# Kernel optimization log

Hardware: AMD Instinct MI355X
Metric: run time of the kernel (lower is better)

The kernel has to match this reference:

```python
import jax, jax.numpy as jnp
import numpy as np

N_STATE = 16
PNAMES = ['in_w', 'conv_w', 'conv_b', 'xproj_w', 'dt_w', 'dt_b', 'A_log', 'D', 'ln_g', 'ln_b', 'out_w']


def _ss2d_params(key, dm, K):
    di = 2 * dm                       # expand = 2
    dr = (dm + 15) // 16              # dt_rank = ceil(d_model/16)
    ks = jax.random.split(key, 6)
    s = lambda k, shape, sc: jax.random.normal(k, shape, jnp.float32) * sc
    cshape = (di, 1, 3, 3) if K == 4 else (di, 1, 3)   # depthwise conv kernel
    return {
        'in_w': s(ks[0], (2 * di, dm), dm ** -0.5),
        'conv_w': s(ks[1], cshape, 0.3),
        'conv_b': jnp.zeros((di,), jnp.float32),
        'xproj_w': s(ks[2], (K, dr + 2 * N_STATE, di), di ** -0.5),
        'dt_w': s(ks[3], (K, di, dr), dr ** -0.5),
        'dt_b': s(ks[4], (K, di), 0.1),
        'A_log': jnp.log(jnp.arange(1, N_STATE + 1, dtype=jnp.float32)) * jnp.ones((K, di, N_STATE), jnp.float32),
        'D': jnp.ones((K, di), jnp.float32),
        'ln_g': jnp.ones((di,), jnp.float32),
        'ln_b': jnp.zeros((di,), jnp.float32),
        'out_w': s(ks[5], (dm, di), di ** -0.5),
    }


def _ln(x, g, b, eps=1e-5):
    m = jnp.mean(x, -1, keepdims=True)
    v = jnp.mean((x - m) ** 2, -1, keepdims=True)
    return (x - m) * jax.lax.rsqrt(v + eps) * g + b


def _scan_branches(xs, p):
    # xs: (B, K, di, L) -- selective scan along L for each direction k
    dr = p['dt_w'].shape[-1]
    x_dbl = jnp.einsum('bkdl,kcd->bkcl', xs, p['xproj_w'])
    dts, Bs, Cs = jnp.split(x_dbl, [dr, dr + N_STATE], axis=2)
    delta = jax.nn.softplus(jnp.einsum('bkrl,kdr->bkdl', dts, p['dt_w']) + p['dt_b'][None, :, :, None])
    A = -jnp.exp(p['A_log'])                               # (K, di, N)
    dA = jnp.exp(jnp.einsum('bkdl,kdn->lbkdn', delta, A))  # time-major for scan
    dBu = jnp.einsum('bkdl,bknl,bkdl->lbkdn', delta, Bs, xs)

    def step(h, io):
        a, bu = io
        h = a * h + bu
        return h, h

    h0 = jnp.zeros(dA.shape[1:], xs.dtype)
    _, hs = jax.lax.scan(step, h0, (dA, dBu))              # (L, B, K, di, N)
    y = jnp.einsum('lbkdn,bknl->bkdl', hs, Cs)
    return y + xs * p['D'][None, :, :, None]


def _ss2d_2d(x, p):
    # VMamba SS2D: x (B, H, W, dm) -> (B, H, W, dm), 4 scan directions
    xz = jnp.einsum('bhwc,ec->bhwe', x, p['in_w'])
    xin, z = jnp.split(xz, 2, -1)
    u = xin.transpose(0, 3, 1, 2)
    u = jax.lax.conv_general_dilated(u, p['conv_w'], (1, 1), 'SAME',
        dimension_numbers=('NCHW', 'OIHW', 'NCHW'), feature_group_count=u.shape[1])
    u = jax.nn.silu(u + p['conv_b'][None, :, None, None])
    Bb, di, H, W = u.shape
    L = H * W
    xf = u.reshape(Bb, di, L)                              # row-major
    xt = u.transpose(0, 1, 3, 2).reshape(Bb, di, L)        # col-major
    xs = jnp.stack([xf, xt, xf[..., ::-1], xt[..., ::-1]], 1)
    ys = _scan_branches(xs, p)                             # (B, 4, di, L)
    y0 = ys[:, 0]
    y2 = ys[:, 2][..., ::-1]
    y1 = ys[:, 1].reshape(Bb, di, W, H).transpose(0, 1, 3, 2).reshape(Bb, di, L)
    y3 = ys[:, 3][..., ::-1].reshape(Bb, di, W, H).transpose(0, 1, 3, 2).reshape(Bb, di, L)
    y = (y0 + y1 + y2 + y3).transpose(0, 2, 1).reshape(Bb, H, W, di)
    y = _ln(y, p['ln_g'], p['ln_b']) * jax.nn.silu(z)
    return jnp.einsum('bhwe,ce->bhwc', y, p['out_w'])


def _ss2d_1d(x, p):
    # SS2D_xb fuse block: x (B, L, dm) -> (B, L, dm), bidirectional 1D scan
    xz = jnp.einsum('blc,ec->ble', x, p['in_w'])
    xin, z = jnp.split(xz, 2, -1)
    u = xin.transpose(0, 2, 1)
    u = jax.lax.conv_general_dilated(u, p['conv_w'], (1,), 'SAME',
        dimension_numbers=('NCH', 'OIH', 'NCH'), feature_group_count=u.shape[1])
    u = jax.nn.silu(u + p['conv_b'][None, :, None])
    xs = jnp.stack([u, u[..., ::-1]], 1)                   # K = 2
    ys = _scan_branches(xs, p)
    y = (ys[:, 0] + ys[:, 1][..., ::-1]).transpose(0, 2, 1)
    y = _ln(y, p['ln_g'], p['ln_b']) * jax.nn.silu(z)
    return jnp.einsum('ble,ce->blc', y, p['out_w'])


def _bridge(C1, C2, C3, p1, p2, p3, pf, n1_g, n1_b):
    y1 = _ss2d_2d(C1.transpose(0, 2, 3, 1), p1).transpose(0, 3, 1, 2)
    y2 = _ss2d_2d(C2.transpose(0, 2, 3, 1), p2).transpose(0, 3, 1, 2)
    y3 = _ss2d_2d(C3.transpose(0, 2, 3, 1), p3).transpose(0, 3, 1, 2)
    B_, C, H, W = y1.shape                                 # C=24, H=W=112
    # faithful RAW reshapes (no permute), exactly as the torch source does
    F1 = y1.reshape(B_, H * W, C)
    F2 = y2.reshape(B_, H * W // 2, C)
    F3 = y3.reshape(B_, H * W // 4, C)
    F = jnp.concatenate([F1, F2, F3], axis=1)              # (B, 21952, 24)
    F = F + _ss2d_1d(_ln(F, n1_g, n1_b), pf)               # dropout = identity (eval)
    o1 = F[:, :12544, :].reshape(B_, C, H, W)
    o2 = F[:, 12544:18816, :].reshape(B_, C * 2, H // 2, W // 2)
    o3 = F[:, 18816:, :].reshape(B_, C * 4, H // 4, W // 4)
    return (o1, o2, o3)


def setup_inputs() -> dict:
    key = jax.random.key(0)
    ks = jax.random.split(key, 7)
    inp = {
        'C1': jax.random.normal(ks[0], (1, 24, 112, 112), jnp.float32),
        'C2': jax.random.normal(ks[1], (1, 48, 56, 56), jnp.float32),
        'C3': jax.random.normal(ks[2], (1, 96, 28, 28), jnp.float32),
    }
    for pfx, dm, K, kk in [('m1', 24, 4, ks[3]), ('m2', 48, 4, ks[4]), ('m3', 96, 4, ks[5]), ('fz', 24, 2, ks[6])]:
        p = _ss2d_params(kk, dm, K)
        for n in PNAMES:
            inp[pfx + '_' + n] = p[n]
    inp['n1_g'] = jnp.ones((24,), jnp.float32)
    inp['n1_b'] = jnp.zeros((24,), jnp.float32)
    return inp


def reference(C1, C2, C3, m1_in_w, m1_conv_w, m1_conv_b, m1_xproj_w, m1_dt_w, m1_dt_b, m1_A_log, m1_D, m1_ln_g, m1_ln_b, m1_out_w, m2_in_w, m2_conv_w, m2_conv_b, m2_xproj_w, m2_dt_w, m2_dt_b, m2_A_log, m2_D, m2_ln_g, m2_ln_b, m2_out_w, m3_in_w, m3_conv_w, m3_conv_b, m3_xproj_w, m3_dt_w, m3_dt_b, m3_A_log, m3_D, m3_ln_g, m3_ln_b, m3_out_w, fz_in_w, fz_conv_w, fz_conv_b, fz_xproj_w, fz_dt_w, fz_dt_b, fz_A_log, fz_D, fz_ln_g, fz_ln_b, fz_out_w, n1_g, n1_b):
    p1 = dict(zip(PNAMES, (m1_in_w, m1_conv_w, m1_conv_b, m1_xproj_w, m1_dt_w, m1_dt_b, m1_A_log, m1_D, m1_ln_g, m1_ln_b, m1_out_w)))
    p2 = dict(zip(PNAMES, (m2_in_w, m2_conv_w, m2_conv_b, m2_xproj_w, m2_dt_w, m2_dt_b, m2_A_log, m2_D, m2_ln_g, m2_ln_b, m2_out_w)))
    p3 = dict(zip(PNAMES, (m3_in_w, m3_conv_w, m3_conv_b, m3_xproj_w, m3_dt_w, m3_dt_b, m3_A_log, m3_D, m3_ln_g, m3_ln_b, m3_out_w)))
    pf = dict(zip(PNAMES, (fz_in_w, fz_conv_w, fz_conv_b, fz_xproj_w, fz_dt_w, fz_dt_b, fz_A_log, fz_D, fz_ln_g, fz_ln_b, fz_out_w)))
    return _bridge(C1, C2, C3, p1, p2, p3, pf, n1_g, n1_b)
```

## Files before the change

### kernel.cpp

```cpp
#include <hip/hip_runtime.h>
#include <hip/hip_bf16.h>
#include <hip/hip_fp16.h>

#define NST 16
#define L2E 1.4426950408889634f

typedef const void* inp;
typedef __half h16;

struct Job {
  inp Cin;
  inp in_w, conv_w, conv_b, xproj_w, dt_w, dt_b, A_log, D, ln_g, ln_b, out_w;
  h16 *u_pre, *z, *u, *delta, *Bs, *Cs, *yg;
  h16 *Hc;
  float *yacc, *Wc, *bc, *Ssum, *A2t, *F0out;
  float *outF; const float* resid;
  const int* aflg;
  int dm, di, dr, K, H, W, L, NCH, CLEN, is2d, TL, CG, PT, cinf;
};
struct Jobs { Job j[4]; int n; const int* dtf; };

__device__ __forceinline__ float ldw(inp p, size_t i, int f32){
  return f32 ? ((const float*)p)[i]
             : __bfloat162float(((const __hip_bfloat16*)p)[i]);
}
__device__ __forceinline__ float hf(const h16* p, size_t i){ return __half2float(p[i]); }
__device__ __forceinline__ float sigm(float x){ return 1.0f/(1.0f + __expf(-x)); }
__device__ __forceinline__ float silu_(float x){ return x * sigm(x); }
__device__ __forceinline__ float softp(float x){ return (x > 20.0f) ? x : __logf(1.0f + __expf(x)); }

__device__ __forceinline__ int map_pos(const Job& J, int k, int l){
  int rev   = J.is2d ? (k >= 2) : (k == 1);
  int trans = J.is2d ? (k & 1) : 0;
  int sl = rev ? (J.L - 1 - l) : l;
  return trans ? ((sl % J.H)*J.W + sl / J.H) : sl;
}

union F4H { float4 f; __half2 h[4]; };

__device__ __forceinline__ void ld16v(const h16* p, float* o){
  const float4* q = (const float4*)p;
  F4H a, b; a.f = q[0]; b.f = q[1];
  #pragma unroll
  for (int i = 0; i < 4; i++){ float2 x = __half22float2(a.h[i]); o[2*i] = x.x; o[2*i+1] = x.y; }
  #pragma unroll
  for (int i = 0; i < 4; i++){ float2 x = __half22float2(b.h[i]); o[8+2*i] = x.x; o[8+2*i+1] = x.y; }
}

__device__ __forceinline__ void ld8v(const h16* p, float* o){
  F4H a; a.f = *(const float4*)p;
  #pragma unroll
  for (int i = 0; i < 4; i++){ float2 x = __half22float2(a.h[i]); o[2*i] = x.x; o[2*i+1] = x.y; }
}

__device__ __forceinline__ void cvt16(float4 a4, float4 b4, float* o){
  F4H a, b; a.f = a4; b.f = b4;
  #pragma unroll
  for (int i = 0; i < 4; i++){ float2 x = __half22float2(a.h[i]); o[2*i] = x.x; o[2*i+1] = x.y; }
  #pragma unroll
  for (int i = 0; i < 4; i++){ float2 x = __half22float2(b.h[i]); o[8+2*i] = x.x; o[8+2*i+1] = x.y; }
}


__global__ void k_detect(const unsigned* D1, int* flag){
  if (threadIdx.x == 0 && blockIdx.x == 0)
    flag[0] = (D1[0] == 0x3F800000u) ? 1 : 0;
}

__global__ void k_wcomb(Jobs js){
  int f32 = *js.dtf;
  int b = blockIdx.x;
  for (int m = 0; m < js.n; m++){
    const Job& J = js.j[m];
    int CC = J.di + 2*NST;
    int CC2 = CC + NST;
    int tot = J.K * CC2 * J.di;
    int nb = (tot + 255) >> 8;
    if (b < nb){
      int t = (b << 8) + (int)threadIdx.x;
      if (t < tot){
        int d = t % J.di; int r = t / J.di; int cout = r % CC2; int k = r / CC2;
        if (cout < J.di){
          float v = 0.0f;
          for (int rr = 0; rr < J.dr; rr++)
            v += ldw(J.dt_w, (size_t)(k*J.di + cout)*J.dr + rr, f32) *
                 ldw(J.xproj_w, (size_t)(k*(J.dr + 2*NST) + rr)*J.di + d, f32);
          J.Wc[(size_t)(k*CC + cout)*J.di + d] = v;
          if (d == 0) J.bc[k*CC + cout] = ldw(J.dt_b, k*J.di + cout, f32);
        } else if (cout < CC){
          int nn = cout - J.di;
          J.Wc[(size_t)(k*CC + cout)*J.di + d] =
            ldw(J.xproj_w, (size_t)(k*(J.dr + 2*NST) + J.dr + nn)*J.di + d, f32);
          if (d == 0) J.bc[k*CC + cout] = 0.0f;
        } else {
          int nn = cout - CC;
          J.A2t[(size_t)(k*NST + nn)*J.di + d] =
            -L2E*__expf(ldw(J.A_log, ((size_t)(k*J.di + d) << 4) + nn, f32));
        }
      }
      return;
    }
    b -= nb;
  }
}

__global__ void k_chkA(Jobs js, int* afl){
  int m = blockIdx.x;
  if (m >= js.n) return;
  const Job& J = js.j[m];
  __shared__ int ok;
  if (threadIdx.x == 0) ok = 1;
  __syncthreads();
  int tot = J.K * NST * J.di;
  int bad = 0;
  for (int t = threadIdx.x; t < tot; t += 256){
    int d = t % J.di; int r = t / J.di; int n = r % NST; int k = r / NST;
    float base = J.A2t[(size_t)(k*NST + 0)*J.di + d];
    float v    = J.A2t[(size_t)(k*NST + n)*J.di + d];
    float expect = (float)(n+1)*base;
    if (fabsf(v - expect) > 1e-4f*fabsf(expect) + 1e-6f) bad = 1;
  }
  if (bad) ok = 0;
  __syncthreads();
  if (threadIdx.x == 0) afl[m] = ok;
}

__global__ void k_inproj(Jobs js){
  int f32 = *js.dtf;
  int b = blockIdx.x;
  for (int m = 0; m < js.n; m++){
    const Job& J = js.j[m];
    int tot = 2*J.di*J.L;
    int nb = (tot + 255) >> 8;
    if (b < nb){
      int cf = J.cinf ? 1 : f32;
      int t = (b << 8) + (int)threadIdx.x;
      if (t < tot){
        int p = t % J.L; int e = t / J.L;
        float acc;
        if (cf && f32){
          const float* Ci = (const float*)J.Cin;
          const float4* w4 = (const float4*)((const float*)J.in_w + (size_t)e*J.dm);
          float a0 = 0.f, a1 = 0.f, a2 = 0.f, a3 = 0.f;
          int n4 = J.dm >> 2;
          for (int c4 = 0; c4 < n4; c4++){
            float4 w = w4[c4];
            int c = c4 << 2;
            a0 = fmaf(Ci[(size_t)(c+0)*J.L + p], w.x, a0);
            a1 = fmaf(Ci[(size_t)(c+1)*J.L + p], w.y, a1);
            a2 = fmaf(Ci[(size_t)(c+2)*J.L + p], w.z, a2);
            a3 = fmaf(Ci[(size_t)(c+3)*J.L + p], w.w, a3);
          }
          acc = (a0+a1)+(a2+a3);
        } else {
          float a0 = 0.f, a1 = 0.f, a2 = 0.f, a3 = 0.f;
          for (int c = 0; c < J.dm; c += 4){
            a0 = fmaf(ldw(J.Cin, (size_t)(c+0)*J.L + p, cf), ldw(J.in_w, (size_t)e*J.dm + c+0, f32), a0);
            a1 = fmaf(ldw(J.Cin, (size_t)(c+1)*J.L + p, cf), ldw(J.in_w, (size_t)e*J.dm + c+1, f32), a1);
            a2 = fmaf(ldw(J.Cin, (size_t)(c+2)*J.L + p, cf), ldw(J.in_w, (size_t)e*J.dm + c+2, f32), a2);
            a3 = fmaf(ldw(J.Cin, (size_t)(c+3)*J.L + p, cf), ldw(J.in_w, (size_t)e*J.dm + c+3, f32), a3);
          }
          acc = (a0+a1)+(a2+a3);
        }
        if (e < J.di) J.u_pre[(size_t)p*J.di + e] = __float2half(acc);
        else          J.z[(size_t)p*J.di + (e - J.di)] = __float2half(acc);
      }
      return;
    }
    b -= nb;
  }
}

__global__ void k_conv(Jobs js){
  int f32 = *js.dtf;
  int b = blockIdx.x;
  for (int m = 0; m < js.n; m++){
    const Job& J = js.j[m];
    int tot = J.L * J.di;
    int nb = (tot + 255) >> 8;
    if (b < nb){
      int t = (b << 8) + (int)threadIdx.x;
      if (t < tot){
        int d = t % J.di; int p = t / J.di;
        float acc = ldw(J.conv_b, d, f32);
        if (J.is2d){
          int h = p / J.W, w = p % J.W;
          for (int kh = 0; kh < 3; kh++){
            int hh = h + kh - 1;
            if ((unsigned)hh < (unsigned)J.H){
              for (int kw = 0; kw < 3; kw++){
                int ww = w + kw - 1;
                if ((unsigned)ww < (unsigned)J.W)
                  acc += ldw(J.conv_w, d*9 + kh*3 + kw, f32) * hf(J.u_pre, (size_t)(hh*J.W + ww)*J.di + d);
              }
            }
          }
        } else {
          for (int kk = 0; kk < 3; kk++){
            int pp = p + kk - 1;
            if ((unsigned)pp < (unsigned)J.L)
              acc += ldw(J.conv_w, d*3 + kk, f32) * hf(J.u_pre, (size_t)pp*J.di + d);
          }
        }
        J.u[(size_t)p*J.di + d] = __float2half(silu_(acc));
      }
      return;
    }
    b -= nb;
  }
}

__global__ void k_deltaBC(Jobs js){
  extern __shared__ float xt[];
  int b = blockIdx.x;
  for (int m = 0; m < js.n; m++){
    const Job& J = js.j[m];
    int TL = J.TL;
    int ntile = (J.L + TL - 1)/TL;
    int nb = J.K * ntile;
    if (b < nb){
      int k = b / ntile, tile = b % ntile;
      int l0 = tile * TL;
      int stride = J.di + 4;
      int d8n = J.di >> 3;
      int VE = TL * d8n;
      for (int idx = threadIdx.x; idx < VE; idx += 256){
        int ll = idx / d8n, d8 = idx % d8n;
        int l = l0 + ll;
        float o[8];
        if (l < J.L){
          ld8v(J.u + (size_t)map_pos(J, k, l)*J.di + (d8 << 3), o);
        } else {
          for (int i = 0; i < 8; i++) o[i] = 0.0f;
        }
        float4* dst = (float4*)(xt + ll*stride + (d8 << 3));
        dst[0] = make_float4(o[0],o[1],o[2],o[3]);
        dst[1] = make_float4(o[4],o[5],o[6],o[7]);
      }
      if (k == 0){
        int lend = l0 + TL; if (lend > J.L) lend = J.L;
        int zt = (lend - l0)*J.di >> 2;
        float4* yz = (float4*)(J.yacc + (size_t)l0*J.di);
        for (int idx = threadIdx.x; idx < zt; idx += 256)
          yz[idx] = make_float4(0.f,0.f,0.f,0.f);
      }
      __syncthreads();
      int CC = J.di + 2*NST;
      int c4n = CC >> 2;
      int NL4 = TL >> 2;
      int items = NL4 * c4n;
      int n4 = J.di >> 2;
      for (int item = threadIdx.x; item < items; item += 256){
        int l4 = item % NL4;
        int cbase = (item / NL4) << 2;
        const float4* w0 = (const float4*)(J.Wc + (size_t)(k*CC + cbase+0)*J.di);
        const float4* w1 = (const float4*)(J.Wc + (size_t)(k*CC + cbase+1)*J.di);
        const float4* w2 = (const float4*)(J.Wc + (size_t)(k*CC + cbase+2)*J.di);
        const float4* w3 = (const float4*)(J.Wc + (size_t)(k*CC + cbase+3)*J.di);
        const float4* x0 = (const float4*)(xt + (l4 + 0*NL4)*stride);
        const float4* x1 = (const float4*)(xt + (l4 + 1*NL4)*stride);
        const float4* x2 = (const float4*)(xt + (l4 + 2*NL4)*stride);
        const float4* x3 = (const float4*)(xt + (l4 + 3*NL4)*stride);
        float acc[4][4];
        #pragma unroll
        for (int j = 0; j < 4; j++){
          acc[j][0]=0.f; acc[j][1]=0.f; acc[j][2]=0.f; acc[j][3]=0.f;
        }
        #pragma unroll 4
        for (int d4 = 0; d4 < n4; d4++){
          float4 W0 = w0[d4], W1 = w1[d4], W2 = w2[d4], W3 = w3[d4];
          float4 X0 = x0[d4], X1 = x1[d4], X2 = x2[d4], X3 = x3[d4];
          #define DOT4(a,X,W) { a = fmaf(X.x,W.x,a); a = fmaf(X.y,W.y,a); a = fmaf(X.z,W.z,a); a = fmaf(X.w,W.w,a); }
          DOT4(acc[0][0],X0,W0) DOT4(acc[0][1],X0,W1) DOT4(acc[0][2],X0,W2) DOT4(acc[0][3],X0,W3)
          DOT4(acc[1][0],X1,W0) DOT4(acc[1][1],X1,W1) DOT4(acc[1][2],X1,W2) DOT4(acc[1][3],X1,W3)
          DOT4(acc[2][0],X2,W0) DOT4(acc[2][1],X2,W1) DOT4(acc[2][2],X2,W2) DOT4(acc[2][3],X2,W3)
          DOT4(acc[3][0],X3,W0) DOT4(acc[3][1],X3,W1) DOT4(acc[3][2],X3,W2) DOT4(acc[3][3],X3,W3)
          #undef DOT4
        }
        float b0 = J.bc[k*CC + cbase+0], b1 = J.bc[k*CC + cbase+1];
        float b2 = J.bc[k*CC + cbase+2], b3 = J.bc[k*CC + cbase+3];
        #pragma unroll
        for (int j = 0; j < 4; j++){
          int l = l0 + l4 + NL4*j;
          if (l >= J.L) continue;
          float av[4] = {acc[j][0]+b0, acc[j][1]+b1, acc[j][2]+b2, acc[j][3]+b3};
          #pragma unroll
          for (int i = 0; i < 4; i++){
            int cout = cbase + i; float v = av[i];
            if (cout < J.di)            J.delta[((size_t)k*J.L + l)*J.di + cout] = __float2half(softp(v));
            else if (cout < J.di + NST) J.Bs[((size_t)k*J.L + l)*NST + (cout - J.di)] = __float2half(v);
            else                        J.Cs[((size_t)k*J.L + l)*NST + (cout - J.di - NST)] = __float2half(v);
          }
        }
      }
      return;
    }
    b -= nb;
  }
}

#define STEPRQ { if (rev){ if(--rm < 0){ rm = J.H - 1; qd--; } } else { if(++rm == J.H){ rm = 0; qd++; } } }

#define HUPD_GEN(S, DX, B) { \
  _Pragma("unroll") \
  for (int n = 0; n < NST; n++) h[n] = fmaf(exp2f((S) * A2[n]), h[n], (DX) * (B)[n]); }
#define HUPDY_GEN(S, DX, B, C, Y) { \
  _Pragma("unroll") \
  for (int n = 0; n < NST; n++){ h[n] = fmaf(exp2f((S) * A2[n]), h[n], (DX) * (B)[n]); (Y) = fmaf(h[n], (C)[n], (Y)); } }

#define POWTREE(Q, P) \
  float P[NST]; \
  P[0]=(Q); P[1]=P[0]*P[0]; P[2]=P[1]*P[0]; P[3]=P[1]*P[1]; \
  P[4]=P[3]*P[0]; P[5]=P[3]*P[1]; P[6]=P[3]*P[2]; P[7]=P[3]*P[3]; \
  P[8]=P[7]*P[0]; P[9]=P[7]*P[1]; P[10]=P[7]*P[2]; P[11]=P[7]*P[3]; \
  P[12]=P[7]*P[4]; P[13]=P[7]*P[5]; P[14]=P[7]*P[6]; P[15]=P[7]*P[7];

#define HUPD_POW(S, DX, B) { \
  float q_ = exp2f((S) * A0); \
  POWTREE(q_, Pw) \
  _Pragma("unroll") \
  for (int n = 0; n < NST; n++) h[n] = fmaf(Pw[n], h[n], (DX) * (B)[n]); }
#define HUPDY_POW(S, DX, B, C, Y) { \
  float q_ = exp2f((S) * A0); \
  POWTREE(q_, Pw) \
  _Pragma("unroll") \
  for (int n = 0; n < NST; n++){ h[n] = fmaf(Pw[n], h[n], (DX) * (B)[n]); (Y) = fmaf(h[n], (C)[n], (Y)); } }

// ... 131 lines not shown
      int SL = J.NCH >> 6;
      int c0 = sid*SL, c1 = c0 + SL;
      float An = J.A2t[(size_t)(k*NST + n)*J.di + d];
      float a = 1.0f, hagg = 0.0f;
      {
        size_t rb = (size_t)(k*J.NCH + c0);
        float ss = J.Ssum[rb*J.di + d];
        h16 hch  = J.Hc[(rb*NST + n)*J.di + d];
        for (int c = c0; c < c1; c++){
          float ssc = ss; h16 hcc = hch;
          if (c + 1 < c1){
            size_t rn = (size_t)(k*J.NCH + c + 1);
            ss  = J.Ssum[rn*J.di + d];
            hch = J.Hc[(rn*NST + n)*J.di + d];
          }
          float P = exp2f(An * ssc);
          hagg = fmaf(P, hagg, __half2float(hcc));
          a *= P;
        }
      }
      sA[sid*17+dd] = a; sH[sid*17+dd] = hagg;
      __syncthreads();
      #pragma unroll
      for (int s = 1; s < 64; s <<= 1){
        float pa = 1.0f, ph = 0.0f;
        if (sid >= s){ pa = sA[(sid-s)*17+dd]; ph = sH[(sid-s)*17+dd]; }
        __syncthreads();
        hagg = fmaf(a, ph, hagg);
        a *= pa;
        sA[sid*17+dd] = a; sH[sid*17+dd] = hagg;
        __syncthreads();
      }
      float Hp = (sid == 0) ? 0.0f : sH[(sid-1)*17+dd];
      {
        size_t rb = (size_t)(k*J.NCH + c0);
        float ss = J.Ssum[rb*J.di + d];
        h16 hch  = J.Hc[(rb*NST + n)*J.di + d];
        for (int c = c0; c < c1; c++){
          float ssc = ss; float hc = __half2float(hch);
          size_t idx = ((size_t)(k*J.NCH + c)*NST + n)*J.di + d;
          if (c + 1 < c1){
            size_t rn = (size_t)(k*J.NCH + c + 1);
            ss  = J.Ssum[rn*J.di + d];
            hch = J.Hc[(rn*NST + n)*J.di + d];
          }
          float P = exp2f(An * ssc);
          J.Hc[idx] = __float2half(Hp);
          Hp = fmaf(P, Hp, hc);
        }
      }
      return;
    }
    b -= nb;
  }
}

__global__ __launch_bounds__(256) void k_passC(Jobs js){
  int f32 = *js.dtf;
  int b = blockIdx.x;
  int wid = (int)threadIdx.x >> 6;
  int lane = (int)threadIdx.x & 63;
  for (int m = 0; m < js.n; m++){
    const Job& J = js.j[m];
    int DG = (J.di + 63) >> 6;
    int units = J.K * J.NCH * DG;
    int nb = (units + 3) >> 2;
    if (b < nb){
      int uu = (b << 2) + wid;
      if (uu >= units) return;
      int afl = *J.aflg;
      int k = uu / (J.NCH * DG);
      int r = uu % (J.NCH * DG);
      int chunk = r / DG, dg = r % DG;
      int d = (dg << 6) + lane;
      if (d >= J.di) return;
      int c0 = chunk * J.CLEN;
      int c1 = c0 + J.CLEN; if (c1 > J.L) c1 = J.L;
      if (c0 >= J.L) return;
      float h[NST];
      size_t sb = (size_t)(k*J.NCH + chunk);
      #pragma unroll
      for (int n = 0; n < NST; n++) h[n] = hf(J.Hc, (sb*NST + n)*J.di + d);
      float Dd = ldw(J.D, k*J.di + d, f32);
      int rev   = J.is2d ? (k >= 2) : (k == 1);
      int trans = J.is2d ? (k & 1) : 0;
      int rm = 0, qd = 0;
      if (trans){
        int sl0 = rev ? (J.L - 1 - c0) : c0;
        qd = sl0 / J.H; rm = sl0 % J.H;
      }
      const h16* dlt = J.delta + ((size_t)k*J.L)*J.di + d;
      const h16* Bb  = J.Bs + ((size_t)k*J.L)*NST;
      const h16* Cb  = J.Cs + ((size_t)k*J.L)*NST;
      if (afl){
        float A0 = J.A2t[(size_t)(k*NST)*J.di + d];
        int l = c0;
        int pos0, pos1 = 0;
        h16 s0h, s1h, x0h, x1h;
        float4 B0a, B0b, B1a, B1b, C0a, C0b, C1a, C1b;
        if (trans){ pos0 = rm*J.W + qd; STEPRQ; } else pos0 = rev ? (J.L-1-l) : l;
        s0h = dlt[(size_t)l*J.di];
        x0h = J.u[(size_t)pos0*J.di + d];
        { const float4* bp = (const float4*)(Bb + (size_t)l*NST); B0a = bp[0]; B0b = bp[1];
          const float4* cp = (const float4*)(Cb + (size_t)l*NST); C0a = cp[0]; C0b = cp[1]; }
        s1h = s0h; x1h = x0h; B1a = B0a; B1b = B0b; C1a = C0a; C1b = C0b;
        if (l + 1 < c1){
          if (trans){ pos1 = rm*J.W + qd; STEPRQ; } else pos1 = rev ? (J.L-2-l) : (l+1);
          s1h = dlt[(size_t)(l+1)*J.di];
          x1h = J.u[(size_t)pos1*J.di + d];
          const float4* bq = (const float4*)(Bb + (size_t)(l+1)*NST); B1a = bq[0]; B1b = bq[1];
          const float4* cq = (const float4*)(Cb + (size_t)(l+1)*NST); C1a = cq[0]; C1b = cq[1];
        }
        while (l < c1){
          int ln = l + 2;
          int np0 = pos0, np1 = pos1;
          h16 ns0 = s0h, ns1 = s1h, nx0 = x0h, nx1 = x1h;
          float4 nB0a = B0a, nB0b = B0b, nB1a = B1a, nB1b = B1b;
          float4 nC0a = C0a, nC0b = C0b, nC1a = C1a, nC1b = C1b;
          if (ln < c1){
            if (trans){ np0 = rm*J.W + qd; STEPRQ; } else np0 = rev ? (J.L-1-ln) : ln;
            ns0 = dlt[(size_t)ln*J.di];
            nx0 = J.u[(size_t)np0*J.di + d];
            { const float4* bp = (const float4*)(Bb + (size_t)ln*NST); nB0a = bp[0]; nB0b = bp[1];
              const float4* cp = (const float4*)(Cb + (size_t)ln*NST); nC0a = cp[0]; nC0b = cp[1]; }
            if (ln + 1 < c1){
              if (trans){ np1 = rm*J.W + qd; STEPRQ; } else np1 = rev ? (J.L-2-ln) : (ln+1);
              ns1 = dlt[(size_t)(ln+1)*J.di];
              nx1 = J.u[(size_t)np1*J.di + d];
              const float4* bq = (const float4*)(Bb + (size_t)(ln+1)*NST); nB1a = bq[0]; nB1b = bq[1];
              const float4* cq = (const float4*)(Cb + (size_t)(ln+1)*NST); nC1a = cq[0]; nC1b = cq[1];
            }
          }
          {
            float s0 = __half2float(s0h), x0 = __half2float(x0h);
            float B0[NST], C0[NST]; cvt16(B0a, B0b, B0); cvt16(C0a, C0b, C0);
            float dx0 = s0 * x0;
            float y0 = 0.0f;
            HUPDY_POW(s0, dx0, B0, C0, y0)
            y0 = fmaf(Dd, x0, y0);
            atomicAdd(&J.yacc[(size_t)pos0*J.di + d], y0);
            if (l + 1 < c1){
              float s1 = __half2float(s1h), x1 = __half2float(x1h);
              float B1[NST], C1[NST]; cvt16(B1a, B1b, B1); cvt16(C1a, C1b, C1);
              float dx1 = s1 * x1;
              float y1 = 0.0f;
              HUPDY_POW(s1, dx1, B1, C1, y1)
              y1 = fmaf(Dd, x1, y1);
              atomicAdd(&J.yacc[(size_t)pos1*J.di + d], y1);
            }
          }
          l = ln; pos0 = np0; pos1 = np1;
          s0h = ns0; s1h = ns1; x0h = nx0; x1h = nx1;
          B0a = nB0a; B0b = nB0b; B1a = nB1a; B1b = nB1b;
          C0a = nC0a; C0b = nC0b; C1a = nC1a; C1b = nC1b;
        }
      } else {
        float A2[NST];
        #pragma unroll
        for (int n = 0; n < NST; n++) A2[n] = J.A2t[(size_t)(k*NST + n)*J.di + d];
        for (int l = c0; l < c1; l++){
          int pos;
          if (trans){ pos = rm*J.W + qd; STEPRQ; } else pos = rev ? (J.L-1-l) : l;
          float s0 = hf(dlt, (size_t)l*J.di);
          float x0 = hf(J.u, (size_t)pos*J.di + d);
          float B0[NST], C0[NST];
          ld16v(Bb + (size_t)l*NST, B0);
          ld16v(Cb + (size_t)l*NST, C0);
          float dx0 = s0 * x0;
          float y0 = 0.0f;
          HUPDY_GEN(s0, dx0, B0, C0, y0)
          y0 = fmaf(Dd, x0, y0);
          atomicAdd(&J.yacc[(size_t)pos*J.di + d], y0);
        }
      }
      return;
    }
    b -= nb;
  }
}

__global__ void k_merge(Jobs js){
  extern __shared__ float sm[];
  const Job& J = js.j[0];
  int f32 = *js.dtf;
  int di = J.di, PT = J.PT;
  int st = di + 1, st2 = di + 2;
  int p0 = blockIdx.x * PT;
  int rows = J.L - p0; if (rows > PT) rows = PT;
  float* ya = sm;
  h16*   zz = (h16*)(sm + (size_t)PT*st);
  float* mres = (float*)(zz + (size_t)PT*st2);
  float* owT = mres + 2*PT;
  int tot = rows*di;
  for (int idx = threadIdx.x; idx < tot; idx += 256){
    int r = idx / di, d = idx % di;
    ya[r*st + d] = J.yacc[(size_t)p0*di + idx];
    zz[r*st2 + d] = J.z[(size_t)p0*di + idx];
  }
  if (J.outF){
    for (int idx = threadIdx.x; idx < J.dm*di; idx += 256){
      int c = idx / di, e = idx % di;
      owT[e*25 + c] = ldw(J.out_w, (size_t)c*di + e, f32);
    }
  }
  __syncthreads();
  int wid = (int)threadIdx.x >> 6, lane = (int)threadIdx.x & 63;
  for (int r = wid; r < rows; r += 4){
    float s = 0.0f, s2 = 0.0f;
    for (int d = lane; d < di; d += 64){
      float v = ya[r*st + d];
      s += v; s2 = fmaf(v, v, s2);
    }
    for (int o = 32; o > 0; o >>= 1){
      s  += __shfl_down(s, o);
      s2 += __shfl_down(s2, o);
    }
    if (lane == 0){
      float mean = s / di;
      float var = s2/di - mean*mean;
      mres[r] = mean;
      mres[PT + r] = rsqrtf(var + 1e-5f);
    }
  }
  __syncthreads();
  if (J.outF){
    {
      int r = (int)threadIdx.x & (PT - 1);
      int dgrp = (int)threadIdx.x / PT;
      int G = 256 / PT;
      if (r < rows){
        float mean = mres[r], rs = mres[PT + r];
        for (int d = dgrp; d < di; d += G){
          float ln = (ya[r*st + d] - mean)*rs*ldw(J.ln_g, d, f32) + ldw(J.ln_b, d, f32);
          ya[r*st + d] = ln * silu_(__half2float(zz[r*st2 + d]));
        }
      }
    }
    __syncthreads();
    for (int idx = threadIdx.x; idx < rows*J.dm; idx += 256){
      int r = idx / J.dm, c = idx % J.dm;
      const float* lr = ya + r*st;
      float acc = 0.0f;
      for (int e = 0; e < di; e += 8){
        #pragma unroll
        for (int j = 0; j < 8; j++)
          acc = fmaf(lr[e+j], owT[(e+j)*25 + c], acc);
      }
      size_t o = (size_t)(p0 + r)*J.dm + c;
      J.outF[o] = J.resid[o] + acc;
    }
  } else {
    int r = (int)threadIdx.x & (PT - 1);
    int dgrp = (int)threadIdx.x / PT;
    int G = 256 / PT;
    if (r < rows){
      float mean = mres[r], rs = mres[PT + r];
      int p = p0 + r;
      for (int d = dgrp; d < di; d += G){
        float ln = (ya[r*st + d] - mean)*rs*ldw(J.ln_g, d, f32) + ldw(J.ln_b, d, f32);
        J.yg[(size_t)d*J.L + p] = __float2half(ln * silu_(__half2float(zz[r*st2 + d])));
      }
    }
  }
}

__global__ void k_outproj(Jobs js){
  int f32 = *js.dtf;
  int b = blockIdx.x;
  for (int m = 0; m < js.n; m++){
    const Job& J = js.j[m];
    int tot = J.dm * J.L;
    int nb = (tot + 255) >> 8;
    if (b < nb){
      int t = (b << 8) + (int)threadIdx.x;
      if (t < tot){
        int p = t % J.L; int c = t / J.L;
        float acc = 0.0f;
        for (int e = 0; e < J.di; e += 8){
          #pragma unroll
          for (int j = 0; j < 8; j++)
            acc = fmaf(hf(J.yg, (size_t)(e+j)*J.L + p),
                       ldw(J.out_w, (size_t)c*J.di + e + j, f32), acc);
        }
        J.F0out[(size_t)c*J.L + p] = acc;
      }
      return;
    }
    b -= nb;
  }
}

__global__ void k_lnrows(const float* F0, inp g, inp bb, float* xt_, int L, int C, const int* dtf){
  __shared__ float sm[256*25];
  int f32 = *dtf;
  int p0 = blockIdx.x * 256;
  int rows = L - p0; if (rows > 256) rows = 256;
  int tot = rows * C;
  for (int idx = threadIdx.x; idx < tot; idx += 256){
    int r = idx / C, c = idx % C;
    sm[r*25 + c] = F0[(size_t)p0*C + idx];
  }
  __syncthreads();
  int r = threadIdx.x;
  if (r < rows){
    const float* row = sm + r*25;
    float s = 0.0f;
    for (int c = 0; c < C; c++) s += row[c];
    float mean = s / C;
    float s2 = 0.0f;
    for (int c = 0; c < C; c++){ float t = row[c]-mean; s2 += t*t; }
    float rs = rsqrtf(s2/C + 1e-5f);
    int p = p0 + r;
    for (int c = 0; c < C; c++)
      xt_[(size_t)c*L + p] = (row[c]-mean)*rs*ldw(g,c,f32) + ldw(bb,c,f32);
  }
}

static inline int cdiv_i(int a, int b){ return (a + b - 1)/b; }

extern "C" void kernel_launch(void* const* d_in, const int* in_sizes, int n_in,
                              void* d_out, int out_size, void* d_ws, size_t ws_size,
                              hipStream_t stream){
  (void)in_sizes; (void)n_in; (void)out_size; (void)ws_size;
  char* base = (char*)d_ws;
  size_t off = 0;
  auto alloc = [&](size_t bytes)->char*{
    off = (off + 255) & ~(size_t)255;
    char* p = base + off; off += bytes; return p;
  };

  int*   dtf = (int*)alloc(4);
  int*   afl = (int*)alloc(4*4);
  float* F0  = (float*)alloc(526848u*4);
  float* Wc1 = (float*)alloc(4u*80*48*4);   float* bc1 = (float*)alloc(4u*80*4);
  float* Wc2 = (float*)alloc(4u*128*96*4);  float* bc2 = (float*)alloc(4u*128*4);
  float* Wc3 = (float*)alloc(4u*224*192*4); float* bc3 = (float*)alloc(4u*224*4);
  float* Wcf = (float*)alloc(2u*80*48*4);   float* bcf = (float*)alloc(2u*80*4);
  float* A21 = (float*)alloc(4u*NST*48*4);
  float* A22 = (float*)alloc(4u*NST*96*4);
  float* A23 = (float*)alloc(4u*NST*192*4);
  float* A2f = (float*)alloc(2u*NST*48*4);
  size_t regionA = off;

  auto fill = [&](Job& J, int pbase, inp Cin, int cinf,
                  int dm, int di, int dr, int K, int H, int W, int L,
                  int NCH, int CLEN, int is2d, int TL, int PT,
                  float* Wc, float* bc, float* A2t, float* F0out){
    J.Cin = Cin; J.cinf = cinf;
    J.in_w    = d_in[pbase+0];
    J.conv_w  = d_in[pbase+1];
    J.conv_b  = d_in[pbase+2];
    J.xproj_w = d_in[pbase+3];
    J.dt_w    = d_in[pbase+4];
    J.dt_b    = d_in[pbase+5];
    J.A_log   = d_in[pbase+6];
    J.D       = d_in[pbase+7];
    J.ln_g    = d_in[pbase+8];
    J.ln_b    = d_in[pbase+9];
    J.out_w   = d_in[pbase+10];
    size_t LD = (size_t)L*di;
    J.yacc  = (float*)alloc(LD*4);
    J.u_pre = (h16*)J.yacc;
    J.z     = (h16*)alloc(LD*2);
    J.u     = (h16*)alloc(LD*2);
    J.yg    = J.u;
    J.delta = (h16*)alloc((size_t)K*LD*2);
    J.Bs    = (h16*)alloc((size_t)K*L*NST*2);
    J.Cs    = (h16*)alloc((size_t)K*L*NST*2);
    J.Hc    = (h16*)alloc((size_t)K*NCH*NST*di*2);
    J.Ssum  = (float*)alloc((size_t)K*NCH*di*4);
    J.Wc = Wc; J.bc = bc; J.A2t = A2t; J.F0out = F0out;
    J.outF = nullptr; J.resid = nullptr;
    J.dm=dm; J.di=di; J.dr=dr; J.K=K; J.H=H; J.W=W; J.L=L; J.NCH=NCH; J.CLEN=CLEN;
    J.is2d=is2d; J.TL=TL; J.CG=256/TL; J.PT=PT;
  };

  Jobs js3; js3.n = 3; js3.dtf = dtf;
  fill(js3.j[0],  3, d_in[0], 0, 24,  48, 2, 4, 112, 112, 12544, 1024, 13, 1, 64, 32, Wc1, bc1, A21, F0);
  fill(js3.j[1], 14, d_in[1], 0, 48,  96, 3, 4,  56,  56,  3136,  256, 13, 1, 32, 32, Wc2, bc2, A22, F0 + 301056);
  fill(js3.j[2], 25, d_in[2], 0, 96, 192, 6, 4,  28,  28,   784,   64, 13, 1, 16, 16, Wc3, bc3, A23, F0 + 451584);
  js3.j[0].aflg = afl + 0;
  js3.j[1].aflg = afl + 1;
  js3.j[2].aflg = afl + 2;

  off = regionA;
  float* xlnT = (float*)alloc(24u*21952*4);
  Jobs js1; js1.n = 1; js1.dtf = dtf;
  fill(js1.j[0], 36, nullptr, 1, 24, 48, 2, 2, 21952, 1, 21952, 2048, 11, 0, 64, 32, Wcf, bcf, A2f, nullptr);
  js1.j[0].Cin = xlnT;
  js1.j[0].aflg = afl + 3;
  js1.j[0].outF = (float*)d_out;
  js1.j[0].resid = F0;

  Jobs js4; js4.n = 4; js4.dtf = dtf;
  js4.j[0] = js3.j[0]; js4.j[1] = js3.j[1]; js4.j[2] = js3.j[2]; js4.j[3] = js1.j[0];

  auto grids = [&](const Jobs& js, int which)->int{
    int g = 0;
    for (int m = 0; m < js.n; m++){
      const Job& J = js.j[m];
      switch (which){
        case 0: g += cdiv_i(J.K*(J.di+3*NST)*J.di, 256); break;
        case 1: g += cdiv_i(2*J.di*J.L, 256); break;
        case 2: g += cdiv_i(J.L*J.di, 256); break;
        case 4: g += cdiv_i(J.K * J.NCH * cdiv_i(J.di, 64), 4); break;
        case 5: g += J.K * NST * (J.di >> 4); break;
        case 7: g += cdiv_i(J.dm*J.L, 256); break;
      }
    }
    return g;
  };

  auto launch_dbc = [&](const Job& Jin){
    Jobs one; one.n = 1; one.dtf = dtf; one.j[0] = Jin;
    const Job& J = one.j[0];
    int grid = J.K * cdiv_i(J.L, J.TL);
    int shm = J.TL*(J.di+4)*4;
    k_deltaBC<<<grid, 256, shm, stream>>>(one);
  };
  auto launch_merge = [&](const Job& Jin){
    Jobs one; one.n = 1; one.dtf = dtf; one.j[0] = Jin;
    const Job& J = one.j[0];
    int grid = cdiv_i(J.L, J.PT);
    int shm = J.PT*(J.di+1)*4 + J.PT*(J.di+2)*2 + 2*J.PT*4 + (J.outF ? 48*25*4 : 0);
    k_merge<<<grid, 256, shm, stream>>>(one);
  };

  k_detect <<<1, 64, 0, stream>>>((const unsigned*)d_in[10], dtf);

  k_wcomb  <<<grids(js4,0), 256, 0, stream>>>(js4);
  k_chkA   <<<4, 256, 0, stream>>>(js4, afl);
  k_inproj <<<grids(js3,1), 256, 0, stream>>>(js3);
  k_conv   <<<grids(js3,2), 256, 0, stream>>>(js3);
  for (int m = 0; m < 3; m++) launch_dbc(js3.j[m]);
  k_passA  <<<grids(js3,4), 256, 0, stream>>>(js3);
  k_passB  <<<grids(js3,5), 1024, 0, stream>>>(js3);
  k_passC  <<<grids(js3,4), 256, 0, stream>>>(js3);
  for (int m = 0; m < 3; m++) launch_merge(js3.j[m]);
  k_outproj<<<grids(js3,7), 256, 0, stream>>>(js3);

  k_lnrows <<<cdiv_i(21952,256), 256, 0, stream>>>(F0, d_in[47], d_in[48], xlnT, 21952, 24, dtf);
  k_inproj <<<grids(js1,1), 256, 0, stream>>>(js1);
  k_conv   <<<grids(js1,2), 256, 0, stream>>>(js1);
  launch_dbc(js1.j[0]);
  k_passA  <<<grids(js1,4), 256, 0, stream>>>(js1);
  k_passB  <<<grids(js1,5), 1024, 0, stream>>>(js1);
  k_passC  <<<grids(js1,4), 256, 0, stream>>>(js1);
  launch_merge(js1.j[0]);
}
```

Before: 520.7 us.

## Fuse LN into in-proj, batch dbc/merge launches, replace scan atomics with per-direction buffers

Folds the A-structure check into k_wcomb using atomicAnd and drops the separate k_chkA launch. Fuses the fusion-block LayerNorm with its input projection into a new k_lnproj kernel. Batches the deltaBC and merge kernels across the three jobs into single launches. The scan now writes per-direction outputs to a K-times larger buffer that merge sums, replacing atomicAdd and the zeroing pass. This cuts launch count and atomic contention at the cost of more memory traffic and footprint for the yacc buffer.

```diff
diff --git a/kernel.cpp b/kernel.cpp
--- a/kernel.cpp
+++ b/kernel.cpp
@@ -62,9 +62,11 @@
 }
 
 
-__global__ void k_detect(const unsigned* D1, int* flag){
-  if (threadIdx.x == 0 && blockIdx.x == 0)
-    flag[0] = (D1[0] == 0x3F800000u) ? 1 : 0;
+__global__ void k_detect(const unsigned* D1, int* flag, int* afl){
+  if (blockIdx.x == 0){
+    if (threadIdx.x == 0) flag[0] = (D1[0] == 0x3F800000u) ? 1 : 0;
+    if (threadIdx.x < 4) afl[threadIdx.x] = 1;
+  }
 }
 
 __global__ void k_wcomb(Jobs js){
@@ -94,35 +96,18 @@
           if (d == 0) J.bc[k*CC + cout] = 0.0f;
         } else {
           int nn = cout - CC;
-          J.A2t[(size_t)(k*NST + nn)*J.di + d] =
-            -L2E*__expf(ldw(J.A_log, ((size_t)(k*J.di + d) << 4) + nn, f32));
+          float v = -L2E*__expf(ldw(J.A_log, ((size_t)(k*J.di + d) << 4) + nn, f32));
+          J.A2t[(size_t)(k*NST + nn)*J.di + d] = v;
+          float base = -L2E*__expf(ldw(J.A_log, ((size_t)(k*J.di + d) << 4), f32));
+          float expect = (float)(nn+1)*base;
+          if (fabsf(v - expect) > 1e-4f*fabsf(expect) + 1e-6f)
+            atomicAnd((int*)J.aflg, 0);
         }
       }
       return;
     }
     b -= nb;
   }
-}
-
-__global__ void k_chkA(Jobs js, int* afl){
-  int m = blockIdx.x;
-  if (m >= js.n) return;
-  const Job& J = js.j[m];
-  __shared__ int ok;
-  if (threadIdx.x == 0) ok = 1;
-  __syncthreads();
-  int tot = J.K * NST * J.di;
-  int bad = 0;
-  for (int t = threadIdx.x; t < tot; t += 256){
-    int d = t % J.di; int r = t / J.di; int n = r % NST; int k = r / NST;
-    float base = J.A2t[(size_t)(k*NST + 0)*J.di + d];
-    float v    = J.A2t[(size_t)(k*NST + n)*J.di + d];
-    float expect = (float)(n+1)*base;
-    if (fabsf(v - expect) > 1e-4f*fabsf(expect) + 1e-6f) bad = 1;
-  }
-  if (bad) ok = 0;
-  __syncthreads();
-  if (threadIdx.x == 0) afl[m] = ok;
 }
 
 __global__ void k_inproj(Jobs js){
@@ -171,6 +156,48 @@
   }
 }
 
+__global__ __launch_bounds__(256) void k_lnproj(const float* F0, inp g, inp bb, inp in_w,
+                                                h16* u_pre, h16* z, int L, const int* dtf){
+  __shared__ float xr[64][25];
+  __shared__ float wsmT[24*96];
+  int f32 = *dtf;
+  int p0 = blockIdx.x << 6;
+  int rows = L - p0; if (rows > 64) rows = 64;
+  for (int i = threadIdx.x; i < 24*96; i += 256){
+    int c = i / 96, e = i % 96;
+    wsmT[i] = ldw(in_w, (size_t)e*24 + c, f32);
+  }
+  for (int idx = threadIdx.x; idx < rows*24; idx += 256){
+    int r = idx / 24, c = idx % 24;
+    xr[r][c] = F0[(size_t)(p0 + r)*24 + c];
+  }
+  __syncthreads();
+  if ((int)threadIdx.x < rows){
+    float* row = xr[threadIdx.x];
+    float s = 0.f;
+    #pragma unroll
+    for (int c = 0; c < 24; c++) s += row[c];
+    float mean = s * (1.0f/24.0f);
+    float s2 = 0.f;
+    #pragma unroll
+    for (int c = 0; c < 24; c++){ float t = row[c]-mean; s2 = fmaf(t,t,s2); }
+    float rs = rsqrtf(s2*(1.0f/24.0f) + 1e-5f);
+    #pragma unroll
+    for (int c = 0; c < 24; c++)
+      row[c] = (row[c]-mean)*rs*ldw(g,c,f32) + ldw(bb,c,f32);
+  }
+  __syncthreads();
+  for (int idx = threadIdx.x; idx < rows*96; idx += 256){
+    int r = idx / 96, e = idx % 96;
+    const float* row = xr[r];
+    float acc = 0.f;
+    #pragma unroll
+    for (int c = 0; c < 24; c++) acc = fmaf(row[c], wsmT[c*96 + e], acc);
+    if (e < 48) u_pre[(size_t)(p0+r)*48 + e] = __float2half(acc);
+    else        z[(size_t)(p0+r)*48 + (e-48)] = __float2half(acc);
+  }
+}
+
 __global__ void k_conv(Jobs js){
   int f32 = *js.dtf;
   int b = blockIdx.x;
@@ -236,13 +263,6 @@
         float4* dst = (float4*)(xt + ll*stride + (d8 << 3));
         dst[0] = make_float4(o[0],o[1],o[2],o[3]);
         dst[1] = make_float4(o[4],o[5],o[6],o[7]);
-      }
-      if (k == 0){
-        int lend = l0 + TL; if (lend > J.L) lend = J.L;
-        int zt = (lend - l0)*J.di >> 2;
-        float4* yz = (float4*)(J.yacc + (size_t)l0*J.di);
-        for (int idx = threadIdx.x; idx < zt; idx += 256)
-          yz[idx] = make_float4(0.f,0.f,0.f,0.f);
       }
       __syncthreads();
       int CC = J.di + 2*NST;
@@ -540,6 +560,7 @@
       #pragma unroll
       for (int n = 0; n < NST; n++) h[n] = hf(J.Hc, (sb*NST + n)*J.di + d);
       float Dd = ldw(J.D, k*J.di + d, f32);
+      float* yk = J.yacc + (size_t)k*J.L*J.di;
       int rev   = J.is2d ? (k >= 2) : (k == 1);
       int trans = J.is2d ? (k & 1) : 0;
       int rm = 0, qd = 0;
@@ -596,7 +617,7 @@
             float y0 = 0.0f;
             HUPDY_POW(s0, dx0, B0, C0, y0)
             y0 = fmaf(Dd, x0, y0);
-            atomicAdd(&J.yacc[(size_t)pos0*J.di + d], y0);
+            yk[(size_t)pos0*J.di + d] = y0;
             if (l + 1 < c1){
               float s1 = __half2float(s1h), x1 = __half2float(x1h);
               float B1[NST], C1[NST]; cvt16(B1a, B1b, B1); cvt16(C1a, C1b, C1);
@@ -604,7 +625,7 @@
               float y1 = 0.0f;
               HUPDY_POW(s1, dx1, B1, C1, y1)
               y1 = fmaf(Dd, x1, y1);
-              atomicAdd(&J.yacc[(size_t)pos1*J.di + d], y1);
+              yk[(size_t)pos1*J.di + d] = y1;
             }
           }
           l = ln; pos0 = np0; pos1 = np1;
@@ -628,7 +649,7 @@
           float y0 = 0.0f;
           HUPDY_GEN(s0, dx0, B0, C0, y0)
           y0 = fmaf(Dd, x0, y0);
-          atomicAdd(&J.yacc[(size_t)pos*J.di + d], y0);
+          yk[(size_t)pos*J.di + d] = y0;
         }
       }
       return;
@@ -639,86 +660,98 @@
 
 __global__ void k_merge(Jobs js){
   extern __shared__ float sm[];
-  const Job& J = js.j[0];
   int f32 = *js.dtf;
-  int di = J.di, PT = J.PT;
-  int st = di + 1, st2 = di + 2;
-  int p0 = blockIdx.x * PT;
-  int rows = J.L - p0; if (rows > PT) rows = PT;
-  float* ya = sm;
-  h16*   zz = (h16*)(sm + (size_t)PT*st);
-  float* mres = (float*)(zz + (size_t)PT*st2);
-  float* owT = mres + 2*PT;
-  int tot = rows*di;
-  for (int idx = threadIdx.x; idx < tot; idx += 256){
-    int r = idx / di, d = idx % di;
-    ya[r*st + d] = J.yacc[(size_t)p0*di + idx];
-    zz[r*st2 + d] = J.z[(size_t)p0*di + idx];
-  }
-  if (J.outF){
-    for (int idx = threadIdx.x; idx < J.dm*di; idx += 256){
-      int c = idx / di, e = idx % di;
-      owT[e*25 + c] = ldw(J.out_w, (size_t)c*di + e, f32);
-    }
-  }
-  __syncthreads();
-  int wid = (int)threadIdx.x >> 6, lane = (int)threadIdx.x & 63;
-  for (int r = wid; r < rows; r += 4){
-    float s = 0.0f, s2 = 0.0f;
-    for (int d = lane; d < di; d += 64){
-      float v = ya[r*st + d];
-      s += v; s2 = fmaf(v, v, s2);
-    }
-    for (int o = 32; o > 0; o >>= 1){
-      s  += __shfl_down(s, o);
-      s2 += __shfl_down(s2, o);
-    }
-    if (lane == 0){
-      float mean = s / di;
-      float var = s2/di - mean*mean;
-      mres[r] = mean;
-      mres[PT + r] = rsqrtf(var + 1e-5f);
-    }
-  }
-  __syncthreads();
-  if (J.outF){
-    {
-      int r = (int)threadIdx.x & (PT - 1);
-      int dgrp = (int)threadIdx.x / PT;
-      int G = 256 / PT;
-      if (r < rows){
-        float mean = mres[r], rs = mres[PT + r];
-        for (int d = dgrp; d < di; d += G){
-          float ln = (ya[r*st + d] - mean)*rs*ldw(J.ln_g, d, f32) + ldw(J.ln_b, d, f32);
-          ya[r*st + d] = ln * silu_(__half2float(zz[r*st2 + d]));
-        }
-      }
-    }
-    __syncthreads();
-    for (int idx = threadIdx.x; idx < rows*J.dm; idx += 256){
-      int r = idx / J.dm, c = idx % J.dm;
-      const float* lr = ya + r*st;
-      float acc = 0.0f;
-      for (int e = 0; e < di; e += 8){
-        #pragma unroll
-        for (int j = 0; j < 8; j++)
-          acc = fmaf(lr[e+j], owT[(e+j)*25 + c], acc);
-      }
-      size_t o = (size_t)(p0 + r)*J.dm + c;
-      J.outF[o] = J.resid[o] + acc;
-    }
-  } else {
-    int r = (int)threadIdx.x & (PT - 1);
-    int dgrp = (int)threadIdx.x / PT;
-    int G = 256 / PT;
-    if (r < rows){
-      float mean = mres[r], rs = mres[PT + r];
-      int p = p0 + r;
-      for (int d = dgrp; d < di; d += G){
-        float ln = (ya[r*st + d] - mean)*rs*ldw(J.ln_g, d, f32) + ldw(J.ln_b, d, f32);
-        J.yg[(size_t)d*J.L + p] = __float2half(ln * silu_(__half2float(zz[r*st2 + d])));
-      }
-    }
+  int b = blockIdx.x;
+  for (int m = 0; m < js.n; m++){
+    const Job& J = js.j[m];
+    int nbk = (J.L + J.PT - 1)/J.PT;
+    if (b < nbk){
+      int di = J.di, PT = J.PT;
+      int st = di + 1, st2 = di + 2;
+      int p0 = b * PT;
+      int rows = J.L - p0; if (rows > PT) rows = PT;
+      float* ya = sm;
+      h16*   zz = (h16*)(sm + (size_t)PT*st);
+      float* mres = (float*)(zz + (size_t)PT*st2);
+      float* owT = mres + 2*PT;
+      size_t LD = (size_t)J.L*di;
+      int tot = rows*di;
+      for (int idx = threadIdx.x; idx < tot; idx += 256){
+        int r = idx / di, d = idx % di;
+        size_t pp = (size_t)p0*di + idx;
+        float v = J.yacc[pp];
+        for (int k = 1; k < J.K; k++) v += J.yacc[(size_t)k*LD + pp];
+        ya[r*st + d] = v;
+        zz[r*st2 + d] = J.z[pp];
+      }
+      if (J.outF){
+        for (int idx = threadIdx.x; idx < J.dm*di; idx += 256){
+          int c = idx / di, e = idx % di;
+          owT[e*25 + c] = ldw(J.out_w, (size_t)c*di + e, f32);
+        }
+      }
+      __syncthreads();
+      int wid = (int)threadIdx.x >> 6, lane = (int)threadIdx.x & 63;
+      for (int r = wid; r < rows; r += 4){
+        float s = 0.0f, s2 = 0.0f;
+        for (int d = lane; d < di; d += 64){
+          float v = ya[r*st + d];
+          s += v; s2 = fmaf(v, v, s2);
+        }
+        for (int o = 32; o > 0; o >>= 1){
+          s  += __shfl_down(s, o);
+          s2 += __shfl_down(s2, o);
+        }
+        if (lane == 0){
+          float mean = s / di;
+          float var = s2/di - mean*mean;
+          mres[r] = mean;
+          mres[PT + r] = rsqrtf(var + 1e-5f);
+        }
+      }
+      __syncthreads();
+      if (J.outF){
+        {
+          int r = (int)threadIdx.x & (PT - 1);
+          int dgrp = (int)threadIdx.x / PT;
+          int G = 256 / PT;
+          if (r < rows){
+            float mean = mres[r], rs = mres[PT + r];
+            for (int d = dgrp; d < di; d += G){
+              float ln = (ya[r*st + d] - mean)*rs*ldw(J.ln_g, d, f32) + ldw(J.ln_b, d, f32);
+              ya[r*st + d] = ln * silu_(__half2float(zz[r*st2 + d]));
+            }
+          }
+        }
+        __syncthreads();
+        for (int idx = threadIdx.x; idx < rows*J.dm; idx += 256){
+          int r = idx / J.dm, c = idx % J.dm;
+          const float* lr = ya + r*st;
+          float acc = 0.0f;
+          for (int e = 0; e < di; e += 8){
+            #pragma unroll
+            for (int j = 0; j < 8; j++)
+              acc = fmaf(lr[e+j], owT[(e+j)*25 + c], acc);
+          }
+          size_t o = (size_t)(p0 + r)*J.dm + c;
+          J.outF[o] = J.resid[o] + acc;
+        }
+      } else {
+        int r = (int)threadIdx.x & (PT - 1);
+        int dgrp = (int)threadIdx.x / PT;
+        int G = 256 / PT;
+        if (r < rows){
+          float mean = mres[r], rs = mres[PT + r];
+          int p = p0 + r;
+          for (int d = dgrp; d < di; d += G){
+            float ln = (ya[r*st + d] - mean)*rs*ldw(J.ln_g, d, f32) + ldw(J.ln_b, d, f32);
+            J.yg[(size_t)d*J.L + p] = __float2half(ln * silu_(__half2float(zz[r*st2 + d])));
+          }
+        }
+      }
+      return;
+    }
+    b -= nbk;
   }
 }
 
@@ -748,32 +781,6 @@
   }
 }
 
-__global__ void k_lnrows(const float* F0, inp g, inp bb, float* xt_, int L, int C, const int* dtf){
-  __shared__ float sm[256*25];
-  int f32 = *dtf;
-  int p0 = blockIdx.x * 256;
-  int rows = L - p0; if (rows > 256) rows = 256;
-  int tot = rows * C;
-  for (int idx = threadIdx.x; idx < tot; idx += 256){
-    int r = idx / C, c = idx % C;
-    sm[r*25 + c] = F0[(size_t)p0*C + idx];
-  }
-  __syncthreads();
-  int r = threadIdx.x;
-  if (r < rows){
-    const float* row = sm + r*25;
-    float s = 0.0f;
-    for (int c = 0; c < C; c++) s += row[c];
-    float mean = s / C;
-    float s2 = 0.0f;
-    for (int c = 0; c < C; c++){ float t = row[c]-mean; s2 += t*t; }
-    float rs = rsqrtf(s2/C + 1e-5f);
-    int p = p0 + r;
-    for (int c = 0; c < C; c++)
-      xt_[(size_t)c*L + p] = (row[c]-mean)*rs*ldw(g,c,f32) + ldw(bb,c,f32);
-  }
-}
-
 static inline int cdiv_i(int a, int b){ return (a + b - 1)/b; }
 
 extern "C" void kernel_launch(void* const* d_in, const int* in_sizes, int n_in,
@@ -817,7 +824,7 @@
     J.ln_b    = d_in[pbase+9];
     J.out_w   = d_in[pbase+10];
     size_t LD = (size_t)L*di;
-    J.yacc  = (float*)alloc(LD*4);
+    J.yacc  = (float*)alloc((size_t)K*LD*4);
     J.u_pre = (h16*)J.yacc;
     J.z     = (h16*)alloc(LD*2);
     J.u     = (h16*)alloc(LD*2);
@@ -842,10 +849,8 @@
   js3.j[2].aflg = afl + 2;
 
   off = regionA;
-  float* xlnT = (float*)alloc(24u*21952*4);
   Jobs js1; js1.n = 1; js1.dtf = dtf;
   fill(js1.j[0], 36, nullptr, 1, 24, 48, 2, 2, 21952, 1, 21952, 2048, 11, 0, 64, 32, Wcf, bcf, A2f, nullptr);
-  js1.j[0].Cin = xlnT;
   js1.j[0].aflg = afl + 3;
   js1.j[0].outF = (float*)d_out;
   js1.j[0].resid = F0;
@@ -861,48 +866,48 @@
         case 0: g += cdiv_i(J.K*(J.di+3*NST)*J.di, 256); break;
         case 1: g += cdiv_i(2*J.di*J.L, 256); break;
         case 2: g += cdiv_i(J.L*J.di, 256); break;
+        case 3: g += J.K * cdiv_i(J.L, J.TL); break;
         case 4: g += cdiv_i(J.K * J.NCH * cdiv_i(J.di, 64), 4); break;
         case 5: g += J.K * NST * (J.di >> 4); break;
+        case 6: g += cdiv_i(J.L, J.PT); break;
         case 7: g += cdiv_i(J.dm*J.L, 256); break;
       }
     }
     return g;
   };
-
-  auto launch_dbc = [&](const Job& Jin){
-    Jobs one; one.n = 1; one.dtf = dtf; one.j[0] = Jin;
-    const Job& J = one.j[0];
-    int grid = J.K * cdiv_i(J.L, J.TL);
-    int shm = J.TL*(J.di+4)*4;
-    k_deltaBC<<<grid, 256, shm, stream>>>(one);
+  auto shm_dbc = [&](const Jobs& js)->int{
+    int s = 0;
+    for (int m = 0; m < js.n; m++){ int v = js.j[m].TL*(js.j[m].di+4)*4; if (v > s) s = v; }
+    return s;
   };
-  auto launch_merge = [&](const Job& Jin){
-    Jobs one; one.n = 1; one.dtf = dtf; one.j[0] = Jin;
-    const Job& J = one.j[0];
-    int grid = cdiv_i(J.L, J.PT);
-    int shm = J.PT*(J.di+1)*4 + J.PT*(J.di+2)*2 + 2*J.PT*4 + (J.outF ? 48*25*4 : 0);
-    k_merge<<<grid, 256, shm, stream>>>(one);
+  auto shm_merge = [&](const Jobs& js)->int{
+    int s = 0;
+    for (int m = 0; m < js.n; m++){
+      const Job& J = js.j[m];
+      int v = J.PT*(J.di+1)*4 + J.PT*(J.di+2)*2 + 2*J.PT*4 + (J.outF ? 48*25*4 : 0);
+      if (v > s) s = v;
+    }
+    return s;
   };
 
-  k_detect <<<1, 64, 0, stream>>>((const unsigned*)d_in[10], dtf);
+  k_detect <<<1, 64, 0, stream>>>((const unsigned*)d_in[10], dtf, afl);
 
   k_wcomb  <<<grids(js4,0), 256, 0, stream>>>(js4);
-  k_chkA   <<<4, 256, 0, stream>>>(js4, afl);
   k_inproj <<<grids(js3,1), 256, 0, stream>>>(js3);
   k_conv   <<<grids(js3,2), 256, 0, stream>>>(js3);
-  for (int m = 0; m < 3; m++) launch_dbc(js3.j[m]);
+  k_deltaBC<<<grids(js3,3), 256, shm_dbc(js3), stream>>>(js3);
   k_passA  <<<grids(js3,4), 256, 0, stream>>>(js3);
   k_passB  <<<grids(js3,5), 1024, 0, stream>>>(js3);
   k_passC  <<<grids(js3,4), 256, 0, stream>>>(js3);
-  for (int m = 0; m < 3; m++) launch_merge(js3.j[m]);
+  k_merge  <<<grids(js3,6), 256, shm_merge(js3), stream>>>(js3);
   k_outproj<<<grids(js3,7), 256, 0, stream>>>(js3);
 
-  k_lnrows <<<cdiv_i(21952,256), 256, 0, stream>>>(F0, d_in[47], d_in[48], xlnT, 21952, 24, dtf);
-  k_inproj <<<grids(js1,1), 256, 0, stream>>>(js1);
+  k_lnproj <<<cdiv_i(21952,64), 256, 0, stream>>>(F0, d_in[47], d_in[48], d_in[36],
+                                                  js1.j[0].u_pre, js1.j[0].z, 21952, dtf);
   k_conv   <<<grids(js1,2), 256, 0, stream>>>(js1);
-  launch_dbc(js1.j[0]);
+  k_deltaBC<<<grids(js1,3), 256, shm_dbc(js1), stream>>>(js1);
   k_passA  <<<grids(js1,4), 256, 0, stream>>>(js1);
   k_passB  <<<grids(js1,5), 1024, 0, stream>>>(js1);
   k_passC  <<<grids(js1,4), 256, 0, stream>>>(js1);
-  launch_merge(js1.j[0]);
-}
+  k_merge  <<<grids(js1,6), 256, shm_merge(js1), stream>>>(js1);
+}
```

Result: faster. 469.0 us (-9.9%).
